# Kernel optimization log

Hardware: AMD Instinct MI355X
Metric: run time of the kernel (lower is better)

The kernel has to match this reference:

```python
import jax, jax.numpy as jnp
import numpy as np
from jax import lax

B, T, C_IN = 64, 1000, 12
D_MODEL, D_STATE, D_CONV, EXPAND = 128, 16, 4, 2
D_INNER = EXPAND * D_MODEL          # 256
DT_RANK = (D_MODEL + 15) // 16      # ceil(d_model/16) = 8
NUM_CLASSES = 5


def setup_inputs() -> dict:
    key = jax.random.key(0)
    ks = jax.random.split(key, 12)
    s = 0.05
    f = jnp.float32
    return {
        "x": jax.random.normal(ks[0], (B, T, C_IN), f),
        # input projection Linear(C_IN, D_MODEL) with bias
        "ip_w": jax.random.normal(ks[1], (D_MODEL, C_IN), f) * s,
        "ip_b": jnp.zeros((D_MODEL,), f),
        # Mamba block params (mamba_ssm layout)
        "in_proj_w": jax.random.normal(ks[2], (2 * D_INNER, D_MODEL), f) * s,
        "conv_w": jax.random.normal(ks[3], (D_INNER, D_CONV), f) * s,
        "conv_b": jnp.zeros((D_INNER,), f),
        "x_proj_w": jax.random.normal(ks[4], (DT_RANK + 2 * D_STATE, D_INNER), f) * s,
        "dt_proj_w": jax.random.normal(ks[5], (D_INNER, DT_RANK), f) * s,
        "dt_proj_b": jax.random.uniform(ks[6], (D_INNER,), f, -4.0, -2.0),  # softplus -> small positive dt
        "A_log": jnp.log(jnp.tile(jnp.arange(1, D_STATE + 1, dtype=f), (D_INNER, 1))),
        "D_skip": jnp.ones((D_INNER,), f),
        "out_proj_w": jax.random.normal(ks[7], (D_MODEL, D_INNER), f) * s,
        # classifier head: Linear(128,64) -> ReLU -> Linear(64,5)
        "fc1_w": jax.random.normal(ks[8], (64, D_MODEL), f) * s,
        "fc1_b": jnp.zeros((64,), f),
        "fc2_w": jax.random.normal(ks[9], (NUM_CLASSES, 64), f) * s,
        "fc2_b": jnp.zeros((NUM_CLASSES,), f),
    }


def _silu(x):
    return x * jax.nn.sigmoid(x)


def _mamba(h, in_proj_w, conv_w, conv_b, x_proj_w, dt_proj_w, dt_proj_b,
           A_log, D_skip, out_proj_w):
    # h: (B, T, D_MODEL)
    xz = h @ in_proj_w.T                              # (B, T, 2*Di)
    xm, z = jnp.split(xz, 2, axis=-1)
    # depthwise causal conv over time (pad left d_conv-1)
    xp = jnp.pad(xm, ((0, 0), (D_CONV - 1, 0), (0, 0)))
    rhs = conv_w.T[:, None, :]                        # (d_conv, 1, Di)
    xc = lax.conv_general_dilated(
        xp, rhs, (1,), 'VALID',
        dimension_numbers=('NHC', 'HIO', 'NHC'),
        feature_group_count=D_INNER) + conv_b
    u = _silu(xc)                                     # (B, T, Di)
    dbc = u @ x_proj_w.T                              # (B, T, dt_rank + 2N)
    dt = dbc[..., :DT_RANK]
    Bm = dbc[..., DT_RANK:DT_RANK + D_STATE]          # (B, T, N)
    Cm = dbc[..., DT_RANK + D_STATE:]                 # (B, T, N)
    delta = jax.nn.softplus(dt @ dt_proj_w.T + dt_proj_b)  # (B, T, Di)
    A = -jnp.exp(A_log)                               # (Di, N)

    def step(hst, inp):
        d_t, b_t, c_t, u_t = inp                      # (B,Di),(B,N),(B,N),(B,Di)
        dA = jnp.exp(d_t[..., None] * A)              # (B, Di, N)
        hst = dA * hst + (d_t * u_t)[..., None] * b_t[:, None, :]
        y_t = jnp.einsum('bdn,bn->bd', hst, c_t)
        return hst, y_t

    h0 = jnp.zeros((h.shape[0], D_INNER, D_STATE), h.dtype)
    _, ys = lax.scan(step, h0, (delta.transpose(1, 0, 2), Bm.transpose(1, 0, 2),
                                Cm.transpose(1, 0, 2), u.transpose(1, 0, 2)))
    y = ys.transpose(1, 0, 2) + u * D_skip            # (B, T, Di)
    y = y * _silu(z)
    return y @ out_proj_w.T                           # (B, T, D_MODEL)


def reference(x, ip_w, ip_b, in_proj_w, conv_w, conv_b, x_proj_w, dt_proj_w,
              dt_proj_b, A_log, D_skip, out_proj_w, fc1_w, fc1_b, fc2_w, fc2_b):
    h = x @ ip_w.T + ip_b                             # (B, T, D_MODEL)
    y = _mamba(h, in_proj_w, conv_w, conv_b, x_proj_w, dt_proj_w, dt_proj_b,
               A_log, D_skip, out_proj_w)
    last = y[:, -1, :]                                # (B, D_MODEL)
    hid = jax.nn.relu(last @ fc1_w.T + fc1_b)
    return hid @ fc2_w.T + fc2_b                      # (B, NUM_CLASSES)
```

## Files before the change

kernel.cpp:

```cpp
#include <hip/hip_runtime.h>
#include <cstddef>

#define T_LEN 1000
#define B_SZ 64
#define C_IN_ 12
#define D_MODEL_ 128
#define D_INNER_ 256
#define D_STATE_ 16
#define DT_RANK_ 8
#define N_CLS 5
#define NCH 10
#define CT4 25

typedef __attribute__((ext_vector_type(8))) short bf16x8;
typedef __attribute__((ext_vector_type(8))) unsigned short u16x8;
typedef __attribute__((ext_vector_type(4))) float f32x4;

__device__ __forceinline__ float fast_exp2(float x) {
#if __has_builtin(__builtin_amdgcn_exp2f)
  return __builtin_amdgcn_exp2f(x);
#else
  float r; asm volatile("v_exp_f32 %0, %1" : "=v"(r) : "v"(x)); return r;
#endif
}
__device__ __forceinline__ float fast_log2(float x) {
#if __has_builtin(__builtin_amdgcn_logf)
  return __builtin_amdgcn_logf(x);
#else
  float r; asm volatile("v_log_f32 %0, %1" : "=v"(r) : "v"(x)); return r;
#endif
}
__device__ __forceinline__ float fast_rcp(float x) {
#if __has_builtin(__builtin_amdgcn_rcpf)
  return __builtin_amdgcn_rcpf(x);
#else
  float r; asm volatile("v_rcp_f32 %0, %1" : "=v"(r) : "v"(x)); return r;
#endif
}
__device__ __forceinline__ float silu_f(float x) {
  float den = 1.f + fast_exp2(-x * 1.4426950408889634f);
  return x * fast_rcp(den);
}
__device__ __forceinline__ float softplus_f(float x) {
  const float L = 1.4426950408889634f, iL = 0.6931471805599453f;
  float e = fast_exp2(-fabsf(x) * L);
  float l = fast_log2(1.f + e) * iL;
  return fmaxf(x, 0.f) + l;
}
__device__ __forceinline__ unsigned short f2bf(float f) {
  unsigned u = __builtin_bit_cast(unsigned, f);
  u = u + 0x7FFFu + ((u >> 16) & 1u);
  return (unsigned short)(u >> 16);
}
__device__ __forceinline__ float bf2f(unsigned short h) {
  unsigned u = ((unsigned)h) << 16;
  return __builtin_bit_cast(float, u);
}

__global__ __launch_bounds__(256) void k0_prep(
    const float* __restrict__ x, const float* __restrict__ ip_w,
    const float* __restrict__ ip_b, const float* __restrict__ in_proj_w,
    char* __restrict__ h_pk, char* __restrict__ w_pk)
{
  __shared__ unsigned short pk_s[8192];
  __shared__ unsigned short pkw_s[32768];
  const int tid = threadIdx.x;

  if (blockIdx.x == 16) {
    if (blockIdx.y != 0) return;
    const int n = tid;
    for (int k = 0; k < D_MODEL_; ++k) {
      unsigned short v = f2bf(in_proj_w[(size_t)n * D_MODEL_ + k]);
      int off = ((n >> 4) * 4 + (k >> 5)) * 512 + ((k & 31) >> 3) * 128
              + (n & 15) * 8 + (k & 7);
      pkw_s[off] = v;
    }
    __syncthreads();
    const float4* s4 = (const float4*)pkw_s;
    float4* dst = (float4*)w_pk;
#pragma unroll
    for (int q = 0; q < 16; ++q) dst[tid * 16 + q] = s4[tid * 16 + q];
    return;
  }

  const int tile4 = blockIdx.x;
  const int b = blockIdx.y;
  const int rl = tid & 63;
  const int kc = (tid >> 6) * 32;
  const int t = tile4 * 64 + rl;

  float xr[C_IN_] = {0.f, 0.f, 0.f, 0.f, 0.f, 0.f, 0.f, 0.f, 0.f, 0.f, 0.f, 0.f};
  const bool valid = (t < T_LEN);
  if (valid) {
    const float4* xp = (const float4*)(x + ((size_t)b * T_LEN + t) * C_IN_);
    float4 v0 = xp[0], v1 = xp[1], v2 = xp[2];
    xr[0] = v0.x; xr[1] = v0.y; xr[2] = v0.z;  xr[3] = v0.w;
    xr[4] = v1.x; xr[5] = v1.y; xr[6] = v1.z;  xr[7] = v1.w;
    xr[8] = v2.x; xr[9] = v2.y; xr[10] = v2.z; xr[11] = v2.w;
  }
  for (int kk = 0; kk < 32; ++kk) {
    const int k = kc + kk;
    unsigned short v = 0;
    if (valid) {
      float acc = ip_b[k];
      const float* wr = ip_w + k * C_IN_;
#pragma unroll
      for (int c = 0; c < C_IN_; ++c) acc += xr[c] * wr[c];
      v = f2bf(acc);
    }
    int off = (rl >> 4) * 2048 + (k >> 5) * 512 + ((k & 31) >> 3) * 128
            + (rl & 15) * 8 + (k & 7);
    pk_s[off] = v;
  }
  __syncthreads();
  const float4* s4 = (const float4*)pk_s;
  float4* dst = (float4*)(h_pk + (size_t)(b * 64 + tile4 * 4) * 4096);
#pragma unroll
  for (int q = 0; q < 4; ++q) dst[tid * 4 + q] = s4[tid * 4 + q];
}

__global__ __launch_bounds__(256) void k1_u(
    const char* __restrict__ h_pk, const char* __restrict__ w_pk,
    const float* __restrict__ conv_w, const float* __restrict__ conv_b,
    float* __restrict__ u_out)
{
  __shared__ float xm[67][260];

  const int tile = blockIdx.x;
  const int b    = blockIdx.y;
  const int t0   = tile * 64;
  const int tid  = threadIdx.x;
  const int w    = tid >> 6;
  const int l    = tid & 63;

  {
    const char* achunk = h_pk + (size_t)(b * 64 + tile * 4 + w) * 4096;
    bf16x8 a0 = *(const bf16x8*)(achunk + 0 * 1024 + l * 16);
    bf16x8 a1 = *(const bf16x8*)(achunk + 1 * 1024 + l * 16);
    bf16x8 a2 = *(const bf16x8*)(achunk + 2 * 1024 + l * 16);
    bf16x8 a3 = *(const bf16x8*)(achunk + 3 * 1024 + l * 16);

    const int row_l = w * 16 + (l >> 4) * 4;
#pragma unroll
    for (int nt = 0; nt < 16; ++nt) {
      const char* wb = w_pk + (size_t)nt * 4096 + l * 16;
      bf16x8 b0 = *(const bf16x8*)(wb + 0 * 1024);
      bf16x8 b1 = *(const bf16x8*)(wb + 1 * 1024);
      bf16x8 b2 = *(const bf16x8*)(wb + 2 * 1024);
      bf16x8 b3 = *(const bf16x8*)(wb + 3 * 1024);
      f32x4 acc = {0.f, 0.f, 0.f, 0.f};
      acc = __builtin_amdgcn_mfma_f32_16x16x32_bf16(a0, b0, acc, 0, 0, 0);
      acc = __builtin_amdgcn_mfma_f32_16x16x32_bf16(a1, b1, acc, 0, 0, 0);
      acc = __builtin_amdgcn_mfma_f32_16x16x32_bf16(a2, b2, acc, 0, 0, 0);
      acc = __builtin_amdgcn_mfma_f32_16x16x32_bf16(a3, b3, acc, 0, 0, 0);
      const int col = nt * 16 + (l & 15);
#pragma unroll
      for (int r = 0; r < 4; ++r)
        xm[3 + row_l + r][col] = acc[r];
    }
  }

  if (tile > 0) {
    const char* hchunk = h_pk + (size_t)(b * 64 + tile * 4 - 1) * 4096;
    bf16x8 ha0 = *(const bf16x8*)(hchunk + 0 * 1024 + l * 16);
    bf16x8 ha1 = *(const bf16x8*)(hchunk + 1 * 1024 + l * 16);
    bf16x8 ha2 = *(const bf16x8*)(hchunk + 2 * 1024 + l * 16);
    bf16x8 ha3 = *(const bf16x8*)(hchunk + 3 * 1024 + l * 16);
#pragma unroll
    for (int q = 0; q < 4; ++q) {
      const int nt = w * 4 + q;
      const char* wb = w_pk + (size_t)nt * 4096 + l * 16;
      bf16x8 b0 = *(const bf16x8*)(wb + 0 * 1024);
      bf16x8 b1 = *(const bf16x8*)(wb + 1 * 1024);
      bf16x8 b2 = *(const bf16x8*)(wb + 2 * 1024);
      bf16x8 b3 = *(const bf16x8*)(wb + 3 * 1024);
      f32x4 acc = {0.f, 0.f, 0.f, 0.f};
      acc = __builtin_amdgcn_mfma_f32_16x16x32_bf16(ha0, b0, acc, 0, 0, 0);
      acc = __builtin_amdgcn_mfma_f32_16x16x32_bf16(ha1, b1, acc, 0, 0, 0);
      acc = __builtin_amdgcn_mfma_f32_16x16x32_bf16(ha2, b2, acc, 0, 0, 0);
      acc = __builtin_amdgcn_mfma_f32_16x16x32_bf16(ha3, b3, acc, 0, 0, 0);
      if (l >= 48) {
        const int col = nt * 16 + (l & 15);
        xm[0][col] = acc[1];
        xm[1][col] = acc[2];
        xm[2][col] = acc[3];
      }
    }
  } else {
#pragma unroll
    for (int r = 0; r < 3; ++r) xm[r][tid] = 0.f;
  }
  __syncthreads();

  {
    const int n = tid;
    const float4 cw = *(const float4*)&conv_w[n * 4];
    const float  cb = conv_b[n];
    float x0 = xm[0][n], x1 = xm[1][n], x2 = xm[2][n];
    for (int i = 0; i < 64; ++i) {
      const int t = t0 + i;
      float x3 = xm[3 + i][n];
      if (t < T_LEN) {
        float s = cb + x0 * cw.x + x1 * cw.y + x2 * cw.z + x3 * cw.w;
        u_out[(((size_t)b * T_LEN + t) << 8) + n] = silu_f(s);
      }
      x0 = x1; x1 = x2; x2 = x3;
    }
  }
}

__global__ __launch_bounds__(256) void k3_delta(
    const float* __restrict__ u, const float* __restrict__ x_proj_w,
    const float* __restrict__ dt_proj_w, const float* __restrict__ dt_proj_b,
    float* __restrict__ delta_T, float* __restrict__ du_T,
    float* __restrict__ pk_bm, float* __restrict__ u_last)
{
  __shared__ __align__(16) float smem[24 * 65 * 4];
  float4 (*xp4)[65] = reinterpret_cast<float4(*)[65]>(smem);
  float* tx = smem;
  __shared__ float dt_s[64][9];
  __shared__ float bm_s[64][17];

  const int row0 = blockIdx.x * 64;
  const int tid = threadIdx.x;

  for (int f = tid; f < 24 * 64; f += 256) {
    int c = f >> 6, k4 = f & 63;
    xp4[c][k4] = *(const float4*)&x_proj_w[(size_t)c * 256 + k4 * 4];
  }
  const float4 w0 = *(const float4*)&dt_proj_w[(size_t)tid * 8];
  const float4 w1 = *(const float4*)&dt_proj_w[(size_t)tid * 8 + 4];
  const float bias = dt_proj_b[tid];
  __syncthreads();

  {
    const int r2 = tid >> 3, cg = tid & 7;
    const int ra = 2 * r2;
    const float4* ua4 = (const float4*)(u + (size_t)(row0 + ra) * 256);
    const float4* ub4 = (const float4*)(u + (size_t)(row0 + ra + 1) * 256);
    float a0 = 0.f, a1 = 0.f, a2 = 0.f, b0 = 0.f, b1 = 0.f, b2 = 0.f;
    for (int k4 = 0; k4 < 64; ++k4) {
      float4 a = ua4[k4], bb = ub4[k4];
      float4 q0 = xp4[cg * 3 + 0][k4];
      float4 q1 = xp4[cg * 3 + 1][k4];
      float4 q2 = xp4[cg * 3 + 2][k4];
      a0 += a.x * q0.x + a.y * q0.y + a.z * q0.z + a.w * q0.w;
      a1 += a.x * q1.x + a.y * q1.y + a.z * q1.z + a.w * q1.w;
      a2 += a.x * q2.x + a.y * q2.y + a.z * q2.z + a.w * q2.w;
      b0 += bb.x * q0.x + bb.y * q0.y + bb.z * q0.z + bb.w * q0.w;
      b1 += bb.x * q1.x + bb.y * q1.y + bb.z * q1.z + bb.w * q1.w;
      b2 += bb.x * q2.x + bb.y * q2.y + bb.z * q2.z + bb.w * q2.w;
    }
    float va[2][3] = {{a0, a1, a2}, {b0, b1, b2}};
#pragma unroll
    for (int rr = 0; rr < 2; ++rr)
#pragma unroll
      for (int c = 0; c < 3; ++c) {
        int col = cg * 3 + c;
        int row = ra + rr;
        if (col < 8) dt_s[row][col] = va[rr][c];
        else bm_s[row][col - 8] = va[rr][c];
      }
  }
  __syncthreads();

  for (int c16 = 0; c16 < 4; ++c16) {
    float dd[16], uu[16];
#pragma unroll
    for (int j = 0; j < 16; ++j) {
      int r = c16 * 16 + j;
      float pre = bias
        + dt_s[r][0] * w0.x + dt_s[r][1] * w0.y + dt_s[r][2] * w0.z + dt_s[r][3] * w0.w
        + dt_s[r][4] * w1.x + dt_s[r][5] * w1.y + dt_s[r][6] * w1.z + dt_s[r][7] * w1.w;
      float dlt = softplus_f(pre);
      size_t o = (size_t)(row0 + r) * 256 + tid;
      float uv = u[o];
      dd[j] = dlt;
      uu[j] = dlt * uv;
      int rowg = row0 + r;
      if ((rowg - (rowg / 1000) * 1000) == 999)
        u_last[(rowg / 1000) * 256 + tid] = uv;
    }
#pragma unroll
    for (int j = 0; j < 16; ++j) tx[tid * 17 + j] = dd[j];
    __syncthreads();
#pragma unroll
    for (int q = 0; q < 4; ++q) {
      int d_ = (tid >> 2) + 64 * q;
      int t4 = (tid & 3) * 4;
      float4 v = make_float4(tx[d_ * 17 + t4], tx[d_ * 17 + t4 + 1],
                             tx[d_ * 17 + t4 + 2], tx[d_ * 17 + t4 + 3]);
      int rowg = row0 + c16 * 16 + t4;
      int bb = rowg / 1000;
      int t = rowg - bb * 1000;
      *(float4*)&delta_T[((size_t)(bb * 256 + d_)) * 1000 + t] = v;
    }
    __syncthreads();
#pragma unroll
    for (int j = 0; j < 16; ++j) tx[tid * 17 + j] = uu[j];
    __syncthreads();
#pragma unroll
    for (int q = 0; q < 4; ++q) {
      int d_ = (tid >> 2) + 64 * q;
      int t4 = (tid & 3) * 4;
      float4 v = make_float4(tx[d_ * 17 + t4], tx[d_ * 17 + t4 + 1],
                             tx[d_ * 17 + t4 + 2], tx[d_ * 17 + t4 + 3]);
      int rowg = row0 + c16 * 16 + t4;
      int bb = rowg / 1000;
      int t = rowg - bb * 1000;
      *(float4*)&du_T[((size_t)(bb * 256 + d_)) * 1000 + t] = v;
    }
    __syncthreads();
  }
  if (tid < 16) {
    for (int g = 0; g < 8; ++g) {
      float pb[8];
#pragma unroll
      for (int j = 0; j < 8; ++j) pb[j] = bm_s[g * 8 + j][tid];
      int row = row0 + g * 8;
      int bb_ = row / 1000;
      int t   = row - bb_ * 1000;
      size_t base = (((size_t)bb_ * 250 + (t >> 2)) * 16 + tid) * 4;
      *(float4*)&pk_bm[base]      = make_float4(pb[0], pb[1], pb[2], pb[3]);
      *(float4*)&pk_bm[base + 64] = make_float4(pb[4], pb[5], pb[6], pb[7]);
    }
  }
}

__global__ __launch_bounds__(256, 4) void k4_scan(
    const float* __restrict__ delta_T, const float* __restrict__ du_T,
    const float* __restrict__ pk_bm, const float* __restrict__ A_log,
    float* __restrict__ Qb, float* __restrict__ Pb)
{
  __shared__ float bs[CT4][16][4];

  const int d0 = blockIdx.x * 16;
  const int b  = blockIdx.y;
  const int c  = blockIdx.z;
  const int tid = threadIdx.x;
  const int dl = tid >> 4;
  const int n  = tid & 15;
  const int d  = d0 + dl;

  {
    const float4* src = (const float4*)(pk_bm + ((size_t)b * 250 + (size_t)c * CT4) * 64);
    float4* dst = (float4*)bs;
    for (int f = tid; f < CT4 * 16; f += 256) dst[f] = src[f];
  }
  const float A2 = -expf(A_log[(size_t)d * 16 + n]) * 1.4426950408889634f;
  const float* dp = delta_T + ((size_t)(b * 256 + d)) * 1000 + c * 100;
  const float* xp = du_T    + ((size_t)(b * 256 + d)) * 1000 + c * 100;
  __syncthreads();

  float s = 0.f, sum = 0.f;
#pragma unroll
  for (int i = 0; i < CT4; ++i) {
    float4 dv = *(const float4*)(dp + 4 * i);
    float4 xv = *(const float4*)(xp + 4 * i);
    float4 bv = *(const float4*)&bs[i][n][0];
    sum += (dv.x + dv.y) + (dv.z + dv.w);
    s = fast_exp2(dv.x * A2) * s + xv.x * bv.x;
    s = fast_exp2(dv.y * A2) * s + xv.y * bv.y;
    s = fast_exp2(dv.z * A2) * s + xv.z * bv.z;
    s = fast_exp2(dv.w * A2) * s + xv.w * bv.w;
  }

  const size_t o = (size_t)c * 262144 + (size_t)b * 4096 + (size_t)d0 * 16 + tid;
  Qb[o] = s;
  Pb[o] = fast_exp2(A2 * sum);
}

__global__ __launch_bounds__(256) void k4b_combine(
    const float* __restrict__ Qb, const float* __restrict__ Pb,
    float* __restrict__ state_out)
{
  const size_t g = (size_t)blockIdx.x * 256 + threadIdx.x;
  float s = Qb[g];
#pragma unroll
  for (int c = 1; c < NCH; ++c)
    s = Qb[(size_t)c * 262144 + g] + Pb[(size_t)c * 262144 + g] * s;
  state_out[g] = s;
}

__global__ __launch_bounds__(256) void k5_head(
    const float* __restrict__ x, const float* __restrict__ ip_w,
    const float* __restrict__ ip_b, const float* __restrict__ in_proj_w,
    const float* __restrict__ x_proj_w, const float* __restrict__ u_last,
    const float* __restrict__ state, const float* __restrict__ D_skip,
    const float* __restrict__ out_proj_w, const float* __restrict__ fc1_w,
    const float* __restrict__ fc1_b, const float* __restrict__ fc2_w,
    const float* __restrict__ fc2_b, float* __restrict__ out)
{
  const int b = blockIdx.x, tid = threadIdx.x;
  __shared__ float hl[128], ul[256], zs[256], cm[16], yv[256], ov[128], hid[64];
  if (tid < 128) {
    float acc = ip_b[tid];
    const float* xr = x + ((size_t)b * T_LEN + (T_LEN - 1)) * C_IN_;
#pragma unroll
    for (int c = 0; c < C_IN_; ++c) acc += xr[c] * ip_w[tid * C_IN_ + c];
    hl[tid] = acc;
  }
  ul[tid] = u_last[b * 256 + tid];
  __syncthreads();
  {
    float acc = 0.f;
    const float4* wv = (const float4*)(in_proj_w + (size_t)(256 + tid) * 128);
    const float4* h4 = (const float4*)hl;
    for (int k = 0; k < 32; ++k) {
      float4 a = wv[k], c = h4[k];
      acc += c.x * a.x + c.y * a.y + c.z * a.z + c.w * a.w;
    }
    zs[tid] = silu_f(acc);
  }
  if (tid < 16) {
    float acc = 0.f;
    const float4* wv = (const float4*)(x_proj_w + (size_t)(24 + tid) * 256);
    const float4* u4 = (const float4*)ul;
    for (int k = 0; k < 64; ++k) {
      float4 a = wv[k], c = u4[k];
      acc += c.x * a.x + c.y * a.y + c.z * a.z + c.w * a.w;
    }
    cm[tid] = acc;
  }
  __syncthreads();
  {
    const float* st = state + ((size_t)b * 256 + tid) * 16;
    float acc = 0.f;
#pragma unroll
    for (int n = 0; n < 16; ++n) acc += st[n] * cm[n];
    yv[tid] = (acc + ul[tid] * D_skip[tid]) * zs[tid];
  }
  __syncthreads();
  if (tid < 128) {
    float acc = 0.f;
    const float4* wv = (const float4*)(out_proj_w + (size_t)tid * 256);
    const float4* y4 = (const float4*)yv;
    for (int k = 0; k < 64; ++k) {
      float4 a = wv[k], c = y4[k];
      acc += c.x * a.x + c.y * a.y + c.z * a.z + c.w * a.w;
    }
    ov[tid] = acc;
  }
  __syncthreads();
  if (tid < 64) {
    float acc = fc1_b[tid];
    const float4* wv = (const float4*)(fc1_w + (size_t)tid * 128);
    const float4* o4 = (const float4*)ov;
    for (int k = 0; k < 32; ++k) {
      float4 a = wv[k], c = o4[k];
      acc += c.x * a.x + c.y * a.y + c.z * a.z + c.w * a.w;
    }
    hid[tid] = fmaxf(acc, 0.f);
  }
  __syncthreads();
  if (tid < N_CLS) {
    float acc = fc2_b[tid];
    const float* wv = fc2_w + (size_t)tid * 64;
    for (int k = 0; k < 64; ++k) acc += hid[k] * wv[k];
    out[b * N_CLS + tid] = acc;
  }
}

extern "C" void kernel_launch(void* const* d_in, const int* in_sizes, int n_in,
                              void* d_out, int out_size, void* d_ws, size_t ws_size,
                              hipStream_t stream) {
  (void)in_sizes; (void)n_in; (void)out_size; (void)ws_size;
  const float* x         = (const float*)d_in[0];
  const float* ip_w      = (const float*)d_in[1];
  const float* ip_b      = (const float*)d_in[2];
  const float* in_proj_w = (const float*)d_in[3];
  const float* conv_w    = (const float*)d_in[4];
  const float* conv_b    = (const float*)d_in[5];
  const float* x_proj_w  = (const float*)d_in[6];
  const float* dt_proj_w = (const float*)d_in[7];
  const float* dt_proj_b = (const float*)d_in[8];
  const float* A_log     = (const float*)d_in[9];
  const float* D_skip    = (const float*)d_in[10];
  const float* out_proj_w= (const float*)d_in[11];
  const float* fc1_w     = (const float*)d_in[12];
  const float* fc1_b     = (const float*)d_in[13];
  const float* fc2_w     = (const float*)d_in[14];
  const float* fc2_b     = (const float*)d_in[15];
  float* out = (float*)d_out;

  float* u       = (float*)d_ws;
  float* delta_T = u + (size_t)16384000;
  float* du_T    = delta_T + (size_t)16384000;
  float* pk_bm   = du_T + (size_t)16384000;
  float* state   = pk_bm + (size_t)1024000;
  float* u_last  = state + (size_t)262144;
  char* h_pk = (char*)delta_T;
  char* w_pk = h_pk + (size_t)64 * 64 * 4096;
  float* Qb  = u;
  float* Pb  = u + (size_t)4000000;

  k0_prep<<<dim3(17, 64), 256, 0, stream>>>(x, ip_w, ip_b, in_proj_w, h_pk, w_pk);
  k1_u<<<dim3(16, 64), 256, 0, stream>>>(h_pk, w_pk, conv_w, conv_b, u);
  k3_delta<<<1000, 256, 0, stream>>>(u, x_proj_w, dt_proj_w, dt_proj_b,
                                     delta_T, du_T, pk_bm, u_last);
  k4_scan<<<dim3(16, 64, NCH), 256, 0, stream>>>(delta_T, du_T, pk_bm, A_log, Qb, Pb);
  k4b_combine<<<1024, 256, 0, stream>>>(Qb, Pb, state);
  k5_head<<<64, 256, 0, stream>>>(x, ip_w, ip_b, in_proj_w, x_proj_w, u_last, state,
                                  D_skip, out_proj_w, fc1_w, fc1_b, fc2_w, fc2_b, out);
}
```

Measured before the change: 203.6 us.

## Scan all 16 states per thread with finer time chunks

New measurement: 284.1 us. 39.6% more time.

```diff
diff --git a/kernel.cpp b/kernel.cpp
--- a/kernel.cpp
+++ b/kernel.cpp
@@ -9,8 +9,9 @@
 #define D_STATE_ 16
 #define DT_RANK_ 8
 #define N_CLS 5
-#define NCH 10
-#define CT4 25
+#define NCH 25
+#define CSTEP 40
+#define CIT 10
 
 typedef __attribute__((ext_vector_type(8))) short bf16x8;
 typedef __attribute__((ext_vector_type(8))) unsigned short u16x8;
@@ -213,7 +214,7 @@
     const float* __restrict__ u, const float* __restrict__ x_proj_w,
     const float* __restrict__ dt_proj_w, const float* __restrict__ dt_proj_b,
     float* __restrict__ delta_T, float* __restrict__ du_T,
-    float* __restrict__ pk_bm, float* __restrict__ u_last)
+    float* __restrict__ bm_plain, float* __restrict__ u_last)
 {
   __shared__ __align__(16) float smem[24 * 65 * 4];
   float4 (*xp4)[65] = reinterpret_cast<float4(*)[65]>(smem);
@@ -312,62 +313,70 @@
     }
     __syncthreads();
   }
-  if (tid < 16) {
-    for (int g = 0; g < 8; ++g) {
-      float pb[8];
-#pragma unroll
-      for (int j = 0; j < 8; ++j) pb[j] = bm_s[g * 8 + j][tid];
-      int row = row0 + g * 8;
-      int bb_ = row / 1000;
-      int t   = row - bb_ * 1000;
-      size_t base = (((size_t)bb_ * 250 + (t >> 2)) * 16 + tid) * 4;
-      *(float4*)&pk_bm[base]      = make_float4(pb[0], pb[1], pb[2], pb[3]);
-      *(float4*)&pk_bm[base + 64] = make_float4(pb[4], pb[5], pb[6], pb[7]);
-    }
-  }
-}
-
-__global__ __launch_bounds__(256, 4) void k4_scan(
+  {
+    int idx = tid * 4;
+    int row = idx >> 4, n0 = idx & 15;
+    float4 v = make_float4(bm_s[row][n0], bm_s[row][n0 + 1],
+                           bm_s[row][n0 + 2], bm_s[row][n0 + 3]);
+    *(float4*)&bm_plain[((size_t)(row0 + row)) * 16 + n0] = v;
+  }
+}
+
+__global__ __launch_bounds__(256) void k4_scan(
     const float* __restrict__ delta_T, const float* __restrict__ du_T,
-    const float* __restrict__ pk_bm, const float* __restrict__ A_log,
+    const float* __restrict__ bm_plain, const float* __restrict__ A_log,
     float* __restrict__ Qb, float* __restrict__ Pb)
 {
-  __shared__ float bs[CT4][16][4];
-
-  const int d0 = blockIdx.x * 16;
-  const int b  = blockIdx.y;
-  const int c  = blockIdx.z;
-  const int tid = threadIdx.x;
-  const int dl = tid >> 4;
-  const int n  = tid & 15;
-  const int d  = d0 + dl;
-
-  {
-    const float4* src = (const float4*)(pk_bm + ((size_t)b * 250 + (size_t)c * CT4) * 64);
+  __shared__ float bs[CSTEP][16];
+
+  const int b = blockIdx.x;
+  const int c = blockIdx.y;
+  const int d = threadIdx.x;
+
+  {
+    const float4* src = (const float4*)(bm_plain + ((size_t)b * 1000 + c * CSTEP) * 16);
     float4* dst = (float4*)bs;
-    for (int f = tid; f < CT4 * 16; f += 256) dst[f] = src[f];
-  }
-  const float A2 = -expf(A_log[(size_t)d * 16 + n]) * 1.4426950408889634f;
-  const float* dp = delta_T + ((size_t)(b * 256 + d)) * 1000 + c * 100;
-  const float* xp = du_T    + ((size_t)(b * 256 + d)) * 1000 + c * 100;
-  __syncthreads();
-
-  float s = 0.f, sum = 0.f;
-#pragma unroll
-  for (int i = 0; i < CT4; ++i) {
+    if (d < CSTEP * 4) dst[d] = src[d];
+  }
+  float A2[16], s[16];
+#pragma unroll
+  for (int n = 0; n < 16; ++n) {
+    A2[n] = -expf(A_log[(size_t)d * 16 + n]) * 1.4426950408889634f;
+    s[n] = 0.f;
+  }
+  const float* dp = delta_T + ((size_t)(b * 256 + d)) * 1000 + c * CSTEP;
+  const float* xp = du_T    + ((size_t)(b * 256 + d)) * 1000 + c * CSTEP;
+  __syncthreads();
+
+  float sum = 0.f;
+#pragma unroll
+  for (int i = 0; i < CIT; ++i) {
     float4 dv = *(const float4*)(dp + 4 * i);
     float4 xv = *(const float4*)(xp + 4 * i);
-    float4 bv = *(const float4*)&bs[i][n][0];
     sum += (dv.x + dv.y) + (dv.z + dv.w);
-    s = fast_exp2(dv.x * A2) * s + xv.x * bv.x;
-    s = fast_exp2(dv.y * A2) * s + xv.y * bv.y;
-    s = fast_exp2(dv.z * A2) * s + xv.z * bv.z;
-    s = fast_exp2(dv.w * A2) * s + xv.w * bv.w;
-  }
-
-  const size_t o = (size_t)c * 262144 + (size_t)b * 4096 + (size_t)d0 * 16 + tid;
-  Qb[o] = s;
-  Pb[o] = fast_exp2(A2 * sum);
+#pragma unroll
+    for (int j = 0; j < 4; ++j) {
+      const float dvj = (j == 0) ? dv.x : (j == 1) ? dv.y : (j == 2) ? dv.z : dv.w;
+      const float xvj = (j == 0) ? xv.x : (j == 1) ? xv.y : (j == 2) ? xv.z : xv.w;
+      const float4* br = (const float4*)&bs[4 * i + j][0];
+      float4 b0 = br[0], b1 = br[1], b2 = br[2], b3 = br[3];
+      float bv[16] = {b0.x, b0.y, b0.z, b0.w, b1.x, b1.y, b1.z, b1.w,
+                      b2.x, b2.y, b2.z, b2.w, b3.x, b3.y, b3.z, b3.w};
+#pragma unroll
+      for (int n = 0; n < 16; ++n)
+        s[n] = fast_exp2(dvj * A2[n]) * s[n] + xvj * bv[n];
+    }
+  }
+
+  const size_t o = ((size_t)c * 64 + b) * 4096 + (size_t)d * 16;
+#pragma unroll
+  for (int n4 = 0; n4 < 4; ++n4) {
+    *(float4*)&Qb[o + n4 * 4] = make_float4(s[n4 * 4], s[n4 * 4 + 1],
+                                            s[n4 * 4 + 2], s[n4 * 4 + 3]);
+    *(float4*)&Pb[o + n4 * 4] = make_float4(
+        fast_exp2(A2[n4 * 4] * sum), fast_exp2(A2[n4 * 4 + 1] * sum),
+        fast_exp2(A2[n4 * 4 + 2] * sum), fast_exp2(A2[n4 * 4 + 3] * sum));
+  }
 }
 
 __global__ __launch_bounds__(256) void k4b_combine(
@@ -486,19 +495,19 @@
   float* u       = (float*)d_ws;
   float* delta_T = u + (size_t)16384000;
   float* du_T    = delta_T + (size_t)16384000;
-  float* pk_bm   = du_T + (size_t)16384000;
-  float* state   = pk_bm + (size_t)1024000;
+  float* bm      = du_T + (size_t)16384000;
+  float* state   = bm + (size_t)1024000;
   float* u_last  = state + (size_t)262144;
   char* h_pk = (char*)delta_T;
   char* w_pk = h_pk + (size_t)64 * 64 * 4096;
   float* Qb  = u;
-  float* Pb  = u + (size_t)4000000;
+  float* Pb  = u + (size_t)8000000;
 
   k0_prep<<<dim3(17, 64), 256, 0, stream>>>(x, ip_w, ip_b, in_proj_w, h_pk, w_pk);
   k1_u<<<dim3(16, 64), 256, 0, stream>>>(h_pk, w_pk, conv_w, conv_b, u);
   k3_delta<<<1000, 256, 0, stream>>>(u, x_proj_w, dt_proj_w, dt_proj_b,
-                                     delta_T, du_T, pk_bm, u_last);
-  k4_scan<<<dim3(16, 64, NCH), 256, 0, stream>>>(delta_T, du_T, pk_bm, A_log, Qb, Pb);
+                                     delta_T, du_T, bm, u_last);
+  k4_scan<<<dim3(64, NCH), 256, 0, stream>>>(delta_T, du_T, bm, A_log, Qb, Pb);
   k4b_combine<<<1024, 256, 0, stream>>>(Qb, Pb, state);
   k5_head<<<64, 256, 0, stream>>>(x, ip_w, ip_b, in_proj_w, x_proj_w, u_last, state,
                                   D_skip, out_proj_w, fc1_w, fc1_b, fc2_w, fc2_b, out);
```
